# Optimization experiments

Measured on AMD Instinct MI355X. Metric: run time of the kernel, lower is better.

The kernel has to match this reference:

```python
import jax, jax.numpy as jnp
import numpy as np

DEG = np.pi / 180.0
H_FOV = (-180.0 * DEG, 180.0 * DEG)   # azimuth fov (rad)
V_FOV = (-3.0 * DEG, 25.0 * DEG)      # elevation fov (rad), phi = -asin(z/r)
W = 2048  # int((h_fov[1]-h_fov[0]) / h_res), h_res = 360/2048 deg
H = 64    # int((v_fov[1]-v_fov[0]) / v_res), v_res = 28/64 deg
B = 8
N = 2_000_000


def setup_inputs() -> dict:
    key = jax.random.key(0)
    k1, k2, k3 = jax.random.split(key, 3)
    # realistic lidar-scale coordinates: wide xy spread, shallow z
    xyz = jax.random.normal(k1, (N, 3), jnp.float32) * jnp.array([30.0, 30.0, 3.0], jnp.float32)
    inten = jax.random.uniform(k2, (N, 1), dtype=jnp.float32)
    bs = jax.random.randint(k3, (N, 1), 0, B).astype(jnp.float32)  # batch idx stored as float col 0
    points = jnp.concatenate([bs, xyz, inten], axis=1)  # [N, 5]
    return {"points": points, "batch_size": B}


def reference(points, batch_size):
    # points: [N, 1+4] = (batch_idx, x, y, z, intensity)
    bs_idx = points[:, 0].astype(jnp.int32)
    xyz = points[:, 1:4]
    extra = points[:, 4:]

    # spherical projection: r, theta (azimuth, cw from +x), phi (elevation, cw from xy-plane)
    r = jnp.linalg.norm(xyz, axis=1, keepdims=True)                      # [N,1]
    theta = -jnp.arctan2(xyz[:, 1], xyz[:, 0])[:, None]                  # [N,1]
    phi = -jnp.arcsin(xyz[:, 2:3] / jnp.maximum(r, 1e-5))                # [N,1]

    u_n = (theta - H_FOV[0]) / (H_FOV[1] - H_FOV[0])                     # [N,1] normed col
    v_n = (phi - V_FOV[0]) / (V_FOV[1] - V_FOV[0])                       # [N,1] normed row

    mask = (u_n[:, 0] >= 0) & (u_n[:, 0] < 1) & (v_n[:, 0] >= 0) & (v_n[:, 0] < 1)

    u = (u_n[:, 0] * W).astype(jnp.int32)
    v = (v_n[:, 0] * H).astype(jnp.int32)
    # route masked-out points to an out-of-bounds index; scatter mode='drop' discards them
    u = jnp.where(mask, u, W)
    v = jnp.where(mask, v, H)

    # use_xyz=True: features = [xyz, rThetaPhi, raw_features] -> channels = 7
    features = jnp.concatenate([xyz, r, theta, phi, extra], axis=1)      # [N,7]

    rv = jnp.zeros((batch_size, H, W, features.shape[1]), points.dtype)
    rv = rv.at[bs_idx, v, u].set(features, mode='drop')
    return jnp.transpose(rv, (0, 3, 1, 2))  # [B, 7, H, W]
```

## Files before the change

kernel.cpp:

```cpp
#include <hip/hip_runtime.h>
#include <math.h>

#define W_IMG 2048
#define H_IMG 64
#define B_IMG 8
#define C_IMG 7
#define HW_IMG (H_IMG * W_IMG)
#define NPIX (B_IMG * HW_IMG)

typedef float v4f __attribute__((ext_vector_type(4)));

__device__ __forceinline__ float F(unsigned u) { return __uint_as_float(u); }
#define FMAF(a,b,c) __builtin_fmaf((a),(b),(c))

__device__ __forceinline__ float glibc_atanf(float x) {
    const float atanhi[4] = {F(0x3eed6338u), F(0x3f490fdau), F(0x3f7b985eu), F(0x3fc90fdau)};
    const float atanlo[4] = {F(0x31ac3769u), F(0x33222168u), F(0x33140fb4u), F(0x33a22168u)};
    const float aT0 = F(0x3eaaaaabu), aT1 = F(0xbe4ccccdu), aT2 = F(0x3e124925u),
                aT3 = F(0xbde38e38u), aT4 = F(0x3dba2e6eu), aT5 = F(0xbd9d8795u),
                aT6 = F(0x3d886b35u), aT7 = F(0xbd6ef16bu), aT8 = F(0x3d4bda59u),
                aT9 = F(0xbd15a221u), aT10 = F(0x3c8569d7u);

    unsigned hx = __float_as_uint(x);
    unsigned ix = hx & 0x7fffffffu;
    if (ix >= 0x4c800000u) {
        if (ix > 0x7f800000u) return x + x;
        float v = __fadd_rn(atanhi[3], atanlo[3]);
        return (hx >> 31) ? -v : v;
    }
    int id;
    float xr = x;
    if (ix < 0x3ee00000u) {
        if (ix < 0x31000000u) return x;
        id = -1;
    } else {
        xr = fabsf(x);
        if (ix < 0x3f980000u) {
            if (ix < 0x3f300000u) {
                id = 0;
                xr = __fdiv_rn(__fsub_rn(__fmul_rn(2.0f, xr), 1.0f),
                               __fadd_rn(2.0f, xr));
            } else {
                id = 1;
                xr = __fdiv_rn(__fsub_rn(xr, 1.0f), __fadd_rn(xr, 1.0f));
            }
        } else {
            if (ix < 0x401c0000u) {
                id = 2;
                xr = __fdiv_rn(__fsub_rn(xr, 1.5f),
                               __fadd_rn(1.0f, __fmul_rn(1.5f, xr)));
            } else {
                id = 3;
                xr = __fdiv_rn(-1.0f, xr);
            }
        }
    }
    float z = __fmul_rn(xr, xr);
    float w = __fmul_rn(z, z);
    float s1 = __fmul_rn(z, __fadd_rn(aT0, __fmul_rn(w, __fadd_rn(aT2,
               __fmul_rn(w, __fadd_rn(aT4, __fmul_rn(w, __fadd_rn(aT6,
               __fmul_rn(w, __fadd_rn(aT8, __fmul_rn(w, aT10)))))))))));
    float s2 = __fmul_rn(w, __fadd_rn(aT1, __fmul_rn(w, __fadd_rn(aT3,
               __fmul_rn(w, __fadd_rn(aT5, __fmul_rn(w, __fadd_rn(aT7,
               __fmul_rn(w, aT9)))))))));
    if (id < 0) return __fsub_rn(x, __fmul_rn(x, __fadd_rn(s1, s2)));
    float zz = __fsub_rn(atanhi[id],
               __fsub_rn(__fsub_rn(__fmul_rn(xr, __fadd_rn(s1, s2)), atanlo[id]), xr));
    return (hx >> 31) ? -zz : zz;
}

__device__ __forceinline__ float glibc_atan2f(float y, float x) {
    const float pi_o_2 = F(0x3fc90fdbu);
    const float pi     = F(0x40490fdbu);
    const float pi_lo  = F(0xb3bbbd2eu);
    unsigned hx = __float_as_uint(x), hy = __float_as_uint(y);
    unsigned ix = hx & 0x7fffffffu, iy = hy & 0x7fffffffu;
    if (ix > 0x7f800000u || iy > 0x7f800000u) return x + y;
    if (hx == 0x3f800000u) return glibc_atanf(y);
    unsigned m = ((hy >> 31) & 1u) | ((hx >> 30) & 2u);
    if (iy == 0) {
        switch (m) {
            case 0: case 1: return y;
            case 2: return pi;
            default: return -pi;
        }
    }
    if (ix == 0) return (m & 1u) ? -pi_o_2 : pi_o_2;
    if (ix == 0x7f800000u) {
        if (iy == 0x7f800000u) {
            switch (m) {
                case 0: return F(0x3f490fdbu);
                case 1: return -F(0x3f490fdbu);
                case 2: return __fmul_rn(3.0f, F(0x3f490fdbu));
                default: return -__fmul_rn(3.0f, F(0x3f490fdbu));
            }
        } else {
            switch (m) {
                case 0: return 0.0f;
                case 1: return -0.0f;
                case 2: return pi;
                default: return -pi;
            }
        }
    }
    if (iy == 0x7f800000u) return (m & 1u) ? -pi_o_2 : pi_o_2;

    int k = ((int)iy - (int)ix) >> 23;
    float z;
    if (k > 26) {
        z = __fadd_rn(pi_o_2, __fmul_rn(0.5f, pi_lo));
        m &= 1u;
    } else if (k < -26 && (hx >> 31)) {
        z = 0.0f;
    } else {
        z = glibc_atanf(fabsf(__fdiv_rn(y, x)));
    }
    switch (m) {
        case 0: return z;
        case 1: return __uint_as_float(__float_as_uint(z) ^ 0x80000000u);
        case 2: return __fsub_rn(pi, __fsub_rn(z, pi_lo));
        default: return __fsub_rn(__fsub_rn(z, pi_lo), pi);
    }
}

#define H0F   ((float)(-3.14159265358979323846))
#define SPANH ((float)( 6.28318530717958647692))
#define V0F   ((float)(-3.0 * 3.14159265358979323846 / 180.0))
#define SPANV ((float)((25.0 * 3.14159265358979323846 / 180.0) - \
                       (-3.0 * 3.14159265358979323846 / 180.0)))
#define RHc   (1.0f / SPANH)
#define RVc   (1.0f / SPANV)

__device__ __forceinline__ float norm_r(float x, float y, float z) {
    return __fsqrt_rn(FMAF(z, z, FMAF(y, y, __fmul_rn(x, x))));
}

__device__ __forceinline__ float atan01(float t) {
    float q = t * t;
    float p =          -0.0117212f;
    p = FMAF(q, p,      0.05265332f);
    p = FMAF(q, p,     -0.11643287f);
    p = FMAF(q, p,      0.19354346f);
    p = FMAF(q, p,     -0.33262347f);
    p = FMAF(q, p,      0.99997726f);
    return t * p;
}

#define MU 0.06f
#define MV 0.025f

__device__ __forceinline__ int resolve_pix(float bsf, float x, float y, float z) {
    float r  = norm_r(x, y, z);
    float zr = __fdiv_rn(z, fmaxf(r, 1e-5f));
    if (zr > 0.05240f || zr < -0.42270f) return -1;

    float ax = fabsf(x), ay = fabsf(y);
    float mx = fmaxf(ax, ay), mn = fminf(ax, ay);
    float t  = (mx > 0.0f) ? (mn * __builtin_amdgcn_rcpf(mx)) : 0.0f;
    float a  = atan01(t);
    if (ay > ax) a = 1.57079632679f - a;
    if (x < 0.0f) a = 3.14159265359f - a;
    float th = (y < 0.0f) ? a : -a;

    float az  = fabsf(zr);
    float arg = az * __builtin_amdgcn_rsqf(FMAF(-zr, zr, 1.0f));
    float pa  = atan01(arg);
    float ph  = (zr >= 0.0f) ? -pa : pa;

    float uf = (th - H0F) * (RHc * (float)W_IMG);
    float vf = (ph - V0F) * (RVc * (float)H_IMG);
    float ulo = floorf(uf - MU), uhi = floorf(uf + MU);
    float vlo = floorf(vf - MV), vhi = floorf(vf + MV);

    int u, v;
    if (ulo == uhi) {
        u = (int)ulo;
    } else {
        float theta = -glibc_atan2f(y, x);
        float u_n = __fmul_rn(__fsub_rn(theta, H0F), RHc);
        if (!(u_n >= 0.0f && u_n < 1.0f)) return -1;
        u = (int)__fmul_rn(u_n, (float)W_IMG);
    }
    if (u < 0 || u >= W_IMG) return -1;

    if (vlo == vhi) {
        v = (int)vlo;
    } else {
        float s   = __fsqrt_rn(FMAF(-zr, zr, 1.0f));
        float d   = __fadd_rn(1.0f, s);
        float phi = -__fmul_rn(2.0f, glibc_atan2f(zr, d));
        float v_n = __fmul_rn(__fsub_rn(phi, V0F), RVc);
        if (!(v_n >= 0.0f && v_n < 1.0f)) return -1;
        v = (int)__fmul_rn(v_n, (float)H_IMG);
    }
    if (v < 0 || v >= H_IMG) return -1;

    return (((int)bsf) * H_IMG + v) * W_IMG + u;
}

#define SC_TPB 256

__global__ void __launch_bounds__(SC_TPB)
scatter_winner(const float* __restrict__ pts, int* __restrict__ winner, int n) {
    const int t = blockIdx.x * blockDim.x + threadIdx.x;

    int rem = n & 3;
    if (t < rem) {
        int i = n - 1 - t;
        const float* q = pts + (size_t)i * 5;
        int pix = resolve_pix(q[0], q[1], q[2], q[3]);
        if (pix >= 0 && winner[pix] < i) atomicMax(&winner[pix], i);
    }

    const int ngrp = n >> 2;
    const int g = ngrp - 1 - t;
    if (g < 0) return;

    const v4f* p4 = (const v4f*)(pts + (size_t)g * 20);
    v4f a0 = p4[0], a1 = p4[1], a2 = p4[2], a3 = p4[3], a4 = p4[4];
    float f[20];
    *(v4f*)(f +  0) = a0;
    *(v4f*)(f +  4) = a1;
    *(v4f*)(f +  8) = a2;
    *(v4f*)(f + 12) = a3;
    *(v4f*)(f + 16) = a4;

    int pix[4], idx[4];
#pragma unroll
    for (int k = 0; k < 4; ++k) {
        idx[k] = 4 * g + k;
        pix[k] = resolve_pix(f[5*k + 0], f[5*k + 1], f[5*k + 2], f[5*k + 3]);
    }

    int wv[4] = {0x7fffffff, 0x7fffffff, 0x7fffffff, 0x7fffffff};
#pragma unroll
    for (int k = 0; k < 4; ++k)
        if (pix[k] >= 0) wv[k] = winner[pix[k]];

#pragma unroll
    for (int k = 0; k < 4; ++k)
        if (pix[k] >= 0 && wv[k] < idx[k]) atomicMax(&winner[pix[k]], idx[k]);
}

__device__ __forceinline__ void fast_angles(float x, float y, float zr,
                                            float* theta, float* phi) {
    float ax = fabsf(x), ay = fabsf(y);
    float mx = fmaxf(ax, ay), mn = fminf(ax, ay);
    float t = (mx > 0.0f) ? (mn / mx) : 0.0f;
    float a = atan01(t);
    if (ay > ax) a = 1.57079632679f - a;
    if (x < 0.0f) a = 3.14159265359f - a;
    *theta = (y < 0.0f) ? a : -a;

    float az  = fabsf(zr);
    float arg = az / __fsqrt_rn(FMAF(-zr, zr, 1.0f));
    float pa  = atan01(arg);
    *phi = (zr >= 0.0f) ? -pa : pa;
}

__global__ void __launch_bounds__(256, 4)
write_output(const float* __restrict__ pts, const int* __restrict__ winner,
             float* __restrict__ out) {
    int t  = blockIdx.x * blockDim.x + threadIdx.x;
    int p0 = t * 4;
    if (p0 >= NPIX) return;

    int4 w4 = *(const int4*)(winner + p0);
    int wis[4] = {w4.x, w4.y, w4.z, w4.w};

    float qx[4], qy[4], qz[4], qi[4];
#pragma unroll
    for (int k = 0; k < 4; ++k) {
        if (wis[k] >= 0) {
            const float* q = pts + (size_t)wis[k] * 5;
            qx[k] = q[1]; qy[k] = q[2]; qz[k] = q[3]; qi[k] = q[4];
        }
    }

    float fc[C_IMG][4];
#pragma unroll
    for (int c = 0; c < C_IMG; ++c)
#pragma unroll
        for (int k = 0; k < 4; ++k) fc[c][k] = 0.f;

#pragma unroll
    for (int k = 0; k < 4; ++k) {
        if (wis[k] >= 0) {
            float x = qx[k], y = qy[k], z = qz[k];
            float r  = norm_r(x, y, z);
            float zr = __fdiv_rn(z, fmaxf(r, 1e-5f));
            float th, ph;
            fast_angles(x, y, zr, &th, &ph);
            fc[0][k] = x; fc[1][k] = y; fc[2][k] = z;
            fc[3][k] = r; fc[4][k] = th; fc[5][k] = ph;
            fc[6][k] = qi[k];
        }
    }

    int b  = p0 >> 17;
    int hw = p0 & (HW_IMG - 1);
    size_t base = (size_t)b * C_IMG * HW_IMG + hw;
#pragma unroll
    for (int c = 0; c < C_IMG; ++c) {
        v4f v = {fc[c][0], fc[c][1], fc[c][2], fc[c][3]};
        __builtin_nontemporal_store(v, (v4f*)(out + base + (size_t)c * HW_IMG));
    }
}

extern "C" void kernel_launch(void* const* d_in, const int* in_sizes, int n_in,
                              void* d_out, int out_size, void* d_ws, size_t ws_size,
                              hipStream_t stream) {
    const float* pts = (const float*)d_in[0];
    int n = in_sizes[0] / 5;
    if (n <= 0) return;
    int* winner = (int*)d_ws;
    float* out = (float*)d_out;

    int ngrp = n >> 2;
    int blocks = (ngrp + SC_TPB - 1) / SC_TPB;
    if (blocks < 1) blocks = 1;
    scatter_winner<<<blocks, SC_TPB, 0, stream>>>(pts, winner, n);

    int pthreads = NPIX / 4;
    write_output<<<(pthreads + 255) / 256, 256, 0, stream>>>(pts, winner, out);
}
```

Measured before the change: 164.9 us.

## Privatize winner array per XCC and max-reduce copies in output pass

The scatter pass now keeps eight copies of the winner index array, one per XCC, chosen by reading the hardware XCC_ID register. Atomics then stay within one die's L2 instead of contending across dies. The output kernel takes the max over the eight copies before gathering features. The scatter also drops the 4-point vectorised load in favour of one point per thread. In exchange, winner-buffer reads rise eightfold and the workspace must be large enough, with a single-copy fallback when it is not. There is no visible initialisation of the extra copies, which would be a correctness risk if the harness does not fill the workspace.

New measurement: 165.4 us. Within noise of the previous version (+0.3%).

```diff
diff --git a/kernel.cpp b/kernel.cpp
--- a/kernel.cpp
+++ b/kernel.cpp
@@ -7,6 +7,7 @@
 #define C_IMG 7
 #define HW_IMG (H_IMG * W_IMG)
 #define NPIX (B_IMG * HW_IMG)
+#define NCOPY 8
 
 typedef float v4f __attribute__((ext_vector_type(4)));
 
@@ -198,48 +199,37 @@
     return (((int)bsf) * H_IMG + v) * W_IMG + u;
 }
 
+__device__ __forceinline__ int xcc_id() {
+    unsigned x;
+    asm volatile("s_getreg_b32 %0, hwreg(HW_REG_XCC_ID)" : "=s"(x));
+    return (int)(x & 7u);
+}
+
 #define SC_TPB 256
 
 __global__ void __launch_bounds__(SC_TPB)
-scatter_winner(const float* __restrict__ pts, int* __restrict__ winner, int n) {
-    const int t = blockIdx.x * blockDim.x + threadIdx.x;
-
-    int rem = n & 3;
-    if (t < rem) {
-        int i = n - 1 - t;
-        const float* q = pts + (size_t)i * 5;
-        int pix = resolve_pix(q[0], q[1], q[2], q[3]);
-        if (pix >= 0 && winner[pix] < i) atomicMax(&winner[pix], i);
-    }
-
-    const int ngrp = n >> 2;
-    const int g = ngrp - 1 - t;
-    if (g < 0) return;
-
-    const v4f* p4 = (const v4f*)(pts + (size_t)g * 20);
-    v4f a0 = p4[0], a1 = p4[1], a2 = p4[2], a3 = p4[3], a4 = p4[4];
-    float f[20];
-    *(v4f*)(f +  0) = a0;
-    *(v4f*)(f +  4) = a1;
-    *(v4f*)(f +  8) = a2;
-    *(v4f*)(f + 12) = a3;
-    *(v4f*)(f + 16) = a4;
-
-    int pix[4], idx[4];
-#pragma unroll
-    for (int k = 0; k < 4; ++k) {
-        idx[k] = 4 * g + k;
-        pix[k] = resolve_pix(f[5*k + 0], f[5*k + 1], f[5*k + 2], f[5*k + 3]);
-    }
-
-    int wv[4] = {0x7fffffff, 0x7fffffff, 0x7fffffff, 0x7fffffff};
-#pragma unroll
-    for (int k = 0; k < 4; ++k)
-        if (pix[k] >= 0) wv[k] = winner[pix[k]];
-
-#pragma unroll
-    for (int k = 0; k < 4; ++k)
-        if (pix[k] >= 0 && wv[k] < idx[k]) atomicMax(&winner[pix[k]], idx[k]);
+scatter_winner8(const float* __restrict__ pts, int* __restrict__ winner, int n) {
+    int t = blockIdx.x * blockDim.x + threadIdx.x;
+    if (t >= n) return;
+    int i = n - 1 - t;
+    const float* q = pts + (size_t)i * 5;
+    int pix = resolve_pix(q[0], q[1], q[2], q[3]);
+    if (pix < 0) return;
+    int* wc = winner + (size_t)xcc_id() * NPIX;
+    if (wc[pix] >= i) return;
+    atomicMax(&wc[pix], i);
+}
+
+__global__ void __launch_bounds__(SC_TPB)
+scatter_winner1(const float* __restrict__ pts, int* __restrict__ winner, int n) {
+    int t = blockIdx.x * blockDim.x + threadIdx.x;
+    if (t >= n) return;
+    int i = n - 1 - t;
+    const float* q = pts + (size_t)i * 5;
+    int pix = resolve_pix(q[0], q[1], q[2], q[3]);
+    if (pix < 0) return;
+    if (winner[pix] >= i) return;
+    atomicMax(&winner[pix], i);
 }
 
 __device__ __forceinline__ void fast_angles(float x, float y, float zr,
@@ -258,14 +248,21 @@
     *phi = (zr >= 0.0f) ? -pa : pa;
 }
 
+template <int NC>
 __global__ void __launch_bounds__(256, 4)
-write_output(const float* __restrict__ pts, const int* __restrict__ winner,
-             float* __restrict__ out) {
+write_output_t(const float* __restrict__ pts, const int* __restrict__ winner,
+               float* __restrict__ out) {
     int t  = blockIdx.x * blockDim.x + threadIdx.x;
     int p0 = t * 4;
     if (p0 >= NPIX) return;
 
     int4 w4 = *(const int4*)(winner + p0);
+#pragma unroll
+    for (int c = 1; c < NC; ++c) {
+        int4 o = *(const int4*)(winner + (size_t)c * NPIX + p0);
+        w4.x = max(w4.x, o.x); w4.y = max(w4.y, o.y);
+        w4.z = max(w4.z, o.z); w4.w = max(w4.w, o.w);
+    }
     int wis[4] = {w4.x, w4.y, w4.z, w4.w};
 
     float qx[4], qy[4], qz[4], qi[4];
@@ -316,11 +313,15 @@
     int* winner = (int*)d_ws;
     float* out = (float*)d_out;
 
-    int ngrp = n >> 2;
-    int blocks = (ngrp + SC_TPB - 1) / SC_TPB;
-    if (blocks < 1) blocks = 1;
-    scatter_winner<<<blocks, SC_TPB, 0, stream>>>(pts, winner, n);
-
+    int blocks = (n + SC_TPB - 1) / SC_TPB;
     int pthreads = NPIX / 4;
-    write_output<<<(pthreads + 255) / 256, 256, 0, stream>>>(pts, winner, out);
-}
+    int pblocks = (pthreads + 255) / 256;
+
+    if (ws_size >= (size_t)NCOPY * NPIX * sizeof(int)) {
+        scatter_winner8<<<blocks, SC_TPB, 0, stream>>>(pts, winner, n);
+        write_output_t<NCOPY><<<pblocks, 256, 0, stream>>>(pts, winner, out);
+    } else {
+        scatter_winner1<<<blocks, SC_TPB, 0, stream>>>(pts, winner, n);
+        write_output_t<1><<<pblocks, 256, 0, stream>>>(pts, winner, out);
+    }
+}
```
